# Optimization experiments

Hardware: AMD Instinct MI355X
Metric: run time of the kernel (lower is better)

## Reference

```python
import jax, jax.numpy as jnp
from jax import lax
import numpy as np

# Model dims (from MambaVisionEncoder defaults + HF MambaConfig defaults)
HIDDEN = 128      # hidden_dim
DEPTH = 4         # num_hidden_layers
INTER = 4 * HIDDEN  # intermediate_size = 512
STATE = 16        # state_size
DT_RANK = 8       # ceil(hidden/16)
KCONV = 4         # conv_kernel
EPS = 1e-5        # layer_norm_epsilon
B_, T_ = 2, 256
C_, H_, W_ = 3, 224, 224
INPUT_DIM = C_ * H_ * W_


def setup_inputs() -> dict:
    key = jax.random.key(0)
    ks = jax.random.split(key, 8)
    s = 0.02
    return {
        "x": jax.random.normal(ks[0], (B_, T_, C_, H_, W_), jnp.float32),
        # torch Linear weights are [out, in]
        "project_w": jax.random.normal(ks[1], (HIDDEN, INPUT_DIM), jnp.float32) * s,
        "project_b": jnp.zeros((HIDDEN,), jnp.float32),
        "in_proj_w": jax.random.normal(ks[2], (DEPTH, 2 * INTER, HIDDEN), jnp.float32) * s,
        "conv_w": jax.random.normal(ks[3], (DEPTH, INTER, KCONV), jnp.float32) * s,
        "conv_b": jnp.zeros((DEPTH, INTER), jnp.float32),
        "x_proj_w": jax.random.normal(ks[4], (DEPTH, DT_RANK + 2 * STATE, INTER), jnp.float32) * s,
        "dt_proj_w": jax.random.normal(ks[5], (DEPTH, INTER, DT_RANK), jnp.float32) * s,
        "dt_proj_b": jnp.zeros((DEPTH, INTER), jnp.float32),
        # S4D-style init: A_log = log(1..N), broadcast over channels
        "A_log": jnp.log(jnp.broadcast_to(jnp.arange(1, STATE + 1, dtype=jnp.float32), (DEPTH, INTER, STATE))),
        "D_ssm": jnp.ones((DEPTH, INTER), jnp.float32),
        "out_proj_w": jax.random.normal(ks[6], (DEPTH, HIDDEN, INTER), jnp.float32) * s,
        "norm_w": jnp.ones((DEPTH, HIDDEN), jnp.float32),
        "norm_f_w": jnp.ones((HIDDEN,), jnp.float32),
    }


def rmsnorm(x, w):
    var = jnp.mean(jnp.square(x), axis=-1, keepdims=True)
    return x * lax.rsqrt(var + EPS) * w


def mamba_mixer(h, ipw, cw, cb, xpw, dtw, dtb, A_log, Dp, opw):
    # h: [B, T, D]
    Bsz, T, _ = h.shape
    proj = jnp.einsum('btd,ed->bte', h, ipw)          # [B, T, 2I]
    hs, gate = jnp.split(proj, 2, axis=-1)
    hs = hs.transpose(0, 2, 1)                         # [B, I, T]
    # causal depthwise conv1d, kernel KCONV
    conv = lax.conv_general_dilated(
        hs, cw[:, None, :], (1,), [(KCONV - 1, 0)],
        dimension_numbers=('NCH', 'OIH', 'NCH'), feature_group_count=INTER)
    hs = jax.nn.silu(conv + cb[None, :, None])         # [B, I, T]
    ssm_in = jnp.einsum('bit,ei->bte', hs, xpw)        # [B, T, dt_rank+2N]
    dt, Bm, Cm = jnp.split(ssm_in, [DT_RANK, DT_RANK + STATE], axis=-1)
    dt = jax.nn.softplus(jnp.einsum('btr,ir->bti', dt, dtw) + dtb)  # [B, T, I]
    A = -jnp.exp(A_log)                                # [I, N]
    u = hs.transpose(0, 2, 1)                          # [B, T, I]
    dA = jnp.exp(dt[..., None] * A[None, None])        # [B, T, I, N]
    dBu = dt[..., None] * Bm[:, :, None, :] * u[..., None]  # [B, T, I, N]

    def step(state, inp):                              # state: [B, I, N]
        dA_t, dBu_t, C_t = inp
        state = dA_t * state + dBu_t
        y_t = jnp.einsum('bin,bn->bi', state, C_t)
        return state, y_t

    init = jnp.zeros((Bsz, INTER, STATE), hs.dtype)
    _, ys = lax.scan(step, init, (dA.transpose(1, 0, 2, 3), dBu.transpose(1, 0, 2, 3), Cm.transpose(1, 0, 2)))
    y = ys.transpose(1, 0, 2)                          # [B, T, I]
    y = (y + u * Dp[None, None, :]) * jax.nn.silu(gate)
    return jnp.einsum('bti,di->btd', y, opw)           # [B, T, D]


def reference(x, project_w, project_b, in_proj_w, conv_w, conv_b, x_proj_w,
              dt_proj_w, dt_proj_b, A_log, D_ssm, out_proj_w, norm_w, norm_f_w):
    B, T = x.shape[0], x.shape[1]
    flat = x.reshape(B, T, -1)                         # [B, T, input_dim]
    h = jnp.einsum('bti,di->btd', flat, project_w) + project_b  # [B, T, HIDDEN]
    for l in range(DEPTH):
        h = h + mamba_mixer(rmsnorm(h, norm_w[l]), in_proj_w[l], conv_w[l], conv_b[l],
                            x_proj_w[l], dt_proj_w[l], dt_proj_b[l], A_log[l],
                            D_ssm[l], out_proj_w[l])
    return rmsnorm(h, norm_f_w)
```

## Files before the change

kernel.cpp:

```cpp
#include <hip/hip_runtime.h>
#include <hip/hip_bf16.h>

#define HIDDEN 128
#define DEPTH 4
#define INTER 512
#define NSTATE 16
#define DT_RANK 8
#define EPS_RMS 1e-5f
#define MTOK 512
#define KIN 150528

typedef __attribute__((ext_vector_type(8))) short bf16x8;
typedef __attribute__((ext_vector_type(4))) float f32x4;

__device__ __forceinline__ unsigned short f2bf(float f) {
  unsigned int u = __builtin_bit_cast(unsigned int, f);
  u += 0x7fffu + ((u >> 16) & 1u);
  return (unsigned short)(u >> 16);
}
__device__ __forceinline__ float silu_f(float x) {
  return x / (1.0f + __expf(-x));
}

__global__ __launch_bounds__(256) void zero_part(float* __restrict__ p)
{
  const size_t i = (size_t)blockIdx.x * 256 + threadIdx.x;
  ((float4*)p)[i] = (float4){0.f, 0.f, 0.f, 0.f};
}

__global__ __launch_bounds__(512) void proj_gemm(
    const float* __restrict__ x, const float* __restrict__ w,
    float* __restrict__ partial)
{
  const int bid = blockIdx.x;
  const int mb = (bid >> 3) & 3;
  const int kb = (bid & 7) + (bid >> 5) * 8;
  const int nchunk = 18 + (kb < 24 ? 1 : 0);
  const int c0 = kb * 18 + (kb < 24 ? kb : 24);

  __shared__ char sm[256 * 256];

  const int tid = threadIdx.x;
  const int lane = tid & 63;
  const int wv = tid >> 6;
  const int wm2 = wv >> 2;
  const int wn4 = wv & 3;
  const int fr = lane & 15;
  const int kq = lane >> 4;
  const int l31 = lane & 31;
  const int rpar = lane >> 5;

  const float* gptr = (wv < 4)
      ? (x + (size_t)(mb * 128 + wv * 32 + rpar) * KIN + l31 * 4)
      : (w + (size_t)((wv - 4) * 32 + rpar) * KIN + l31 * 4);

  f32x4 acc[4][2];
  #pragma unroll
  for (int mi = 0; mi < 4; ++mi) {
    acc[mi][0] = (f32x4){0.f, 0.f, 0.f, 0.f};
    acc[mi][1] = (f32x4){0.f, 0.f, 0.f, 0.f};
  }

  float4 rv[16];
  {
    const float* base = gptr + (size_t)c0 * 128;
    #pragma unroll
    for (int j = 0; j < 16; ++j)
      rv[j] = *(const float4*)(base + (size_t)(j * 2) * KIN);
  }

  for (int cc = 0; cc < nchunk; ++cc) {
    #pragma unroll
    for (int j = 0; j < 16; ++j) {
      const int r = wv * 32 + j * 2 + rpar;
      const int phys = (l31 * 8) ^ ((r & 7) << 4);
      ushort4 bq = {f2bf(rv[j].x), f2bf(rv[j].y), f2bf(rv[j].z), f2bf(rv[j].w)};
      *(ushort4*)(sm + r * 256 + phys) = bq;
    }
    __syncthreads();
    if (cc + 1 < nchunk) {
      const float* base = gptr + (size_t)(c0 + cc + 1) * 128;
      #pragma unroll
      for (int j = 0; j < 16; ++j)
        rv[j] = *(const float4*)(base + (size_t)(j * 2) * KIN);
    }
    #pragma unroll
    for (int ks = 0; ks < 4; ++ks) {
      const int log = ks * 64 + kq * 16;
      bf16x8 a[4];
      #pragma unroll
      for (int mi = 0; mi < 4; ++mi) {
        const int row = wm2 * 64 + mi * 16 + fr;
        a[mi] = *(const bf16x8*)(sm + row * 256 + (log ^ ((row & 7) << 4)));
      }
      #pragma unroll
      for (int ni = 0; ni < 2; ++ni) {
        const int row = 128 + wn4 * 32 + ni * 16 + fr;
        const bf16x8 b = *(const bf16x8*)(sm + row * 256 + (log ^ ((row & 7) << 4)));
        #pragma unroll
        for (int mi = 0; mi < 4; ++mi)
          acc[mi][ni] = __builtin_amdgcn_mfma_f32_16x16x32_bf16(a[mi], b, acc[mi][ni], 0, 0, 0);
      }
    }
    __syncthreads();
  }
  float* hp = partial + (size_t)(kb & 15) * (MTOK * HIDDEN);
  #pragma unroll
  for (int mi = 0; mi < 4; ++mi)
    #pragma unroll
    for (int ni = 0; ni < 2; ++ni)
      #pragma unroll
      for (int r = 0; r < 4; ++r) {
        const int row = mb * 128 + wm2 * 64 + mi * 16 + kq * 4 + r;
        const int col = wn4 * 32 + ni * 16 + fr;
        atomicAdd(hp + (size_t)row * HIDDEN + col, acc[mi][ni][r]);
      }
}

__global__ __launch_bounds__(512) void fusedA(
    int mode,
    const float* __restrict__ part, const float* __restrict__ pb,
    const float* __restrict__ y_g, const float* __restrict__ gate_g,
    float* __restrict__ h_g,
    const float* __restrict__ opw,
    const float* __restrict__ nw,
    const float* __restrict__ ipw,
    float* __restrict__ hs_g, float* __restrict__ gate_out,
    float* __restrict__ dout)
{
  const int m0 = blockIdx.x * 2;
  const int tid = threadIdx.x;
  const int o2 = tid >> 1;
  const int half = tid & 1;
  const int t = o2 >> 7, d = o2 & 127;
  __shared__ float y2[2][512];
  __shared__ float hrow[2][128];
  __shared__ float hn[2][128];

  float hv;
  if (mode == 0) {
    hv = pb[d];
    #pragma unroll
    for (int s = 0; s < 16; ++s)
      hv += part[(size_t)s * (MTOK * HIDDEN) + (size_t)(m0 + t) * 128 + d];
  } else {
    #pragma unroll
    for (int j = 0; j < 2; ++j) {
      const int o = tid + j * 512;
      const int tt = o >> 9, i = o & 511;
      const float yv = y_g[(size_t)(m0 + tt) * 512 + i];
      const float g  = gate_g[(size_t)(m0 + tt) * 512 + i];
      y2[tt][i] = yv * silu_f(g);
    }
    __syncthreads();
    const float4* yp = (const float4*)(&y2[t][0] + half * 256);
    const float4* wp = (const float4*)(opw + (size_t)d * 512 + half * 256);
    float a0 = 0.f, a1 = 0.f, a2 = 0.f, a3 = 0.f;
    #pragma unroll 8
    for (int kk = 0; kk < 64; ++kk) {
      const float4 yv = yp[kk], wv4 = wp[kk];
      a0 += yv.x * wv4.x; a1 += yv.y * wv4.y;
      a2 += yv.z * wv4.z; a3 += yv.w * wv4.w;
    }
    float a = (a0 + a1) + (a2 + a3);
    a += __shfl_xor(a, 1);
    hv = h_g[(size_t)(m0 + t) * 128 + d] + a;
  }
  if (mode != 2 && half == 0) h_g[(size_t)(m0 + t) * 128 + d] = hv;
  if (half == 0) hrow[t][d] = hv;
  __syncthreads();
  {
    const int wvi = tid >> 6, ln = tid & 63;
    const int tt = wvi & 1;
    const float v0 = hrow[tt][ln], v1 = hrow[tt][ln + 64];
    float ss = v0 * v0 + v1 * v1;
    #pragma unroll
    for (int off = 1; off < 64; off <<= 1) ss += __shfl_xor(ss, off);
    const float rr = rsqrtf(ss * (1.0f / 128.0f) + EPS_RMS);
    if (mode == 2) {
      if (wvi < 2) {
        dout[(size_t)(m0 + tt) * 128 + ln]      = v0 * rr * nw[ln];
        dout[(size_t)(m0 + tt) * 128 + ln + 64] = v1 * rr * nw[ln + 64];
      }
      return;
    }
    if (wvi < 2) {
      hn[tt][ln]      = v0 * rr * nw[ln];
      hn[tt][ln + 64] = v1 * rr * nw[ln + 64];
    }
  }
  __syncthreads();
  #pragma unroll
  for (int j = 0; j < 4; ++j) {
    const int o = tid + j * 512;
    const int tt = o >> 10, e = o & 1023;
    const float4* hp4 = (const float4*)&hn[tt][0];
    const float4* wp4 = (const float4*)(ipw + (size_t)e * 128);
    float a0 = 0.f, a1 = 0.f, a2 = 0.f, a3 = 0.f;
    #pragma unroll
    for (int kk = 0; kk < 32; ++kk) {
      const float4 hvv = hp4[kk], wv4 = wp4[kk];
      a0 += hvv.x * wv4.x; a1 += hvv.y * wv4.y;
      a2 += hvv.z * wv4.z; a3 += hvv.w * wv4.w;
    }
    const float a = (a0 + a1) + (a2 + a3);
    if (e < 512) hs_g[(size_t)(m0 + tt) * 512 + e] = a;
    else         gate_out[(size_t)(m0 + tt) * 512 + (e - 512)] = a;
  }
}

__global__ __launch_bounds__(512) void convxp(
    const float* __restrict__ hs_g, const float* __restrict__ cw,
    const float* __restrict__ cb, const float* __restrict__ xpw,
    const float* __restrict__ dtw, const float* __restrict__ dtb,
    float* __restrict__ uT, float* __restrict__ dtT,
    float* __restrict__ Bm, float* __restrict__ Cm)
{
  const int m0 = blockIdx.x * 2;
  const int b = m0 >> 8, tb0 = m0 & 255;
  const int tid = threadIdx.x;
  __shared__ float hs5[5][512];
  __shared__ float u4[2][512];
  __shared__ float si[2][40];
  for (int o = tid; o < 2560; o += 512) {
    const int j = o >> 9, i = o & 511;
    const int ct = tb0 - 3 + j;
    hs5[j][i] = (ct >= 0) ? hs_g[((size_t)b * 256 + ct) * 512 + i] : 0.f;
  }
  __syncthreads();
  #pragma unroll
  for (int j = 0; j < 2; ++j) {
    const int o = tid + j * 512;
    const int t = o >> 9, i = o & 511;
    const float4 c4v = *(const float4*)(cw + (size_t)i * 4);
    const float s = cb[i] + c4v.x * hs5[t][i] + c4v.y * hs5[t + 1][i]
                          + c4v.z * hs5[t + 2][i] + c4v.w * hs5[t + 3][i];
    const float uu = silu_f(s);
    u4[t][i] = uu;
    uT[((size_t)b * 512 + i) * 256 + tb0 + t] = uu;
  }
  __syncthreads();
  if (tid < 160) {
    const int pid = tid >> 1, half = tid & 1;
    const int t = pid / 40, e = pid % 40;
    const float4* up = (const float4*)(&u4[t][0] + half * 256);
    const float4* wp = (const float4*)(xpw + (size_t)e * 512 + half * 256);
    float a0 = 0.f, a1 = 0.f, a2 = 0.f, a3 = 0.f;
    #pragma unroll 8
    for (int kk = 0; kk < 64; ++kk) {
      const float4 uv = up[kk], wv4 = wp[kk];
      a0 += uv.x * wv4.x; a1 += uv.y * wv4.y;
      a2 += uv.z * wv4.z; a3 += uv.w * wv4.w;
    }
    float a = (a0 + a1) + (a2 + a3);
    a += __shfl_xor(a, 1);
    if (half == 0) si[t][e] = a;
  }
  __syncthreads();
  if (tid < 64) {
    const int t = tid >> 5, q = tid & 31;
    if (q < 16) Bm[(size_t)(m0 + t) * 16 + q] = si[t][8 + q];
    else        Cm[(size_t)(m0 + t) * 16 + (q - 16)] = si[t][24 + (q - 16)];
  }
  #pragma unroll
  for (int j = 0; j < 2; ++j) {
    const int o = tid + j * 512;
    const int i = o >> 1, t = o & 1;
    float a0 = dtb[i];
    const float* dr = dtw + (size_t)i * 8;
    #pragma unroll
    for (int r = 0; r < 8; ++r) a0 += si[t][r] * dr[r];
    const float sp = (a0 > 20.f) ? a0 : log1pf(__expf(a0));
    dtT[((size_t)b * 512 + i) * 256 + tb0 + t] = sp;
  }
}

__global__ __launch_bounds__(256) void scan_k(
    const float* __restrict__ uT, const float* __restrict__ dtT,
    const float* __restrict__ Bm, const float* __restrict__ Cm,
    const float* __restrict__ Alog, const float* __restrict__ Dssm,
    float* __restrict__ y_g)
{
  const int blk = blockIdx.x;
  const int b = blk >> 9, i = blk & 511;
  const int tid = threadIdx.x;
  __shared__ float dt_r[256], u_r[256];
  __shared__ float B_l[256][17], C_l[256][17];
  __shared__ float e_l[16][17], P_l[16][17];
  dt_r[tid] = dtT[((size_t)b * 512 + i) * 256 + tid];
  u_r[tid]  = uT[((size_t)b * 512 + i) * 256 + tid];
  #pragma unroll
  for (int j = 0; j < 16; ++j) {
    const int o = tid + j * 256;
    B_l[o >> 4][o & 15] = Bm[(size_t)b * 4096 + o];
    C_l[o >> 4][o & 15] = Cm[(size_t)b * 4096 + o];
  }
  __syncthreads();
  const int c = tid >> 4, n = tid & 15;
  const float Av = -__expf(Alog[(size_t)i * 16 + n]);
  const float Dv = Dssm[i];
  float aj[16], xj[16];
  float s = 0.f, P = 1.f;
  #pragma unroll
  for (int j = 0; j < 16; ++j) {
    const int t = c * 16 + j;
    const float dtv = dt_r[t];
    const float a = __expf(Av * dtv);
    const float xx = dtv * B_l[t][n] * u_r[t];
    aj[j] = a; xj[j] = xx;
    s = a * s + xx; P *= a;
  }
  e_l[c][n] = s; P_l[c][n] = P;
  __syncthreads();
  float s0 = 0.f;
  for (int cc = 0; cc < c; ++cc)
    s0 = P_l[cc][n] * s0 + e_l[cc][n];
  s = s0;
  #pragma unroll
  for (int j = 0; j < 16; ++j) {
    const int t = c * 16 + j;
    s = aj[j] * s + xj[j];
    float p = s * C_l[t][n];
    p += __shfl_xor(p, 1); p += __shfl_xor(p, 2);
    p += __shfl_xor(p, 4); p += __shfl_xor(p, 8);
    if (n == 0)
      y_g[((size_t)b * 256 + t) * 512 + i] = p + u_r[t] * Dv;
  }
}

extern "C" void kernel_launch(void* const* d_in, const int* in_sizes, int n_in,
                              void* d_out, int out_size, void* d_ws, size_t ws_size,
                              hipStream_t stream)
{
  (void)in_sizes; (void)n_in; (void)out_size; (void)ws_size;
  const float* x    = (const float*)d_in[0];
  const float* pw   = (const float*)d_in[1];
  const float* pb   = (const float*)d_in[2];
  const float* ipw  = (const float*)d_in[3];
  const float* cw   = (const float*)d_in[4];
  const float* cb   = (const float*)d_in[5];
  const float* xpw  = (const float*)d_in[6];
  const float* dtw  = (const float*)d_in[7];
  const float* dtb  = (const float*)d_in[8];
  const float* Alog = (const float*)d_in[9];
  const float* Dssm = (const float*)d_in[10];
  const float* opw  = (const float*)d_in[11];
  const float* nw   = (const float*)d_in[12];
  const float* nwf  = (const float*)d_in[13];
  float* out = (float*)d_out;

  float* ws   = (float*)d_ws;
  float* part = ws;
  float* h    = part + 16 * 65536;
  float* hs   = h + 65536;
  float* gate = hs + 262144;
  float* uT   = gate + 262144;
  float* dtT  = uT + 262144;
  float* Bm   = dtT + 262144;
  float* Cm   = Bm + 8192;
  float* y    = Cm + 8192;

  zero_part<<<dim3(1024), 256, 0, stream>>>(part);
  proj_gemm<<<dim3(256), 512, 0, stream>>>(x, pw, part);

  fusedA<<<dim3(256), 512, 0, stream>>>(0, part, pb, nullptr, nullptr, h,
                                        nullptr, nw, ipw, hs, gate, nullptr);
  for (int l = 0; l < DEPTH; ++l) {
    convxp<<<dim3(256), 512, 0, stream>>>(
        hs, cw + (size_t)l * 2048, cb + (size_t)l * 512,
        xpw + (size_t)l * 40 * 512, dtw + (size_t)l * 512 * 8,
        dtb + (size_t)l * 512, uT, dtT, Bm, Cm);
    scan_k<<<dim3(1024), 256, 0, stream>>>(
        uT, dtT, Bm, Cm, Alog + (size_t)l * 512 * 16, Dssm + (size_t)l * 512, y);
    if (l < DEPTH - 1)
      fusedA<<<dim3(256), 512, 0, stream>>>(1, nullptr, nullptr, y, gate, h,
          opw + (size_t)l * 128 * 512, nw + (size_t)(l + 1) * 128,
          ipw + (size_t)(l + 1) * 1024 * 128, hs, gate, nullptr);
    else
      fusedA<<<dim3(256), 512, 0, stream>>>(2, nullptr, nullptr, y, gate, h,
          opw + (size_t)l * 128 * 512, nwf, nullptr, nullptr, nullptr, out);
  }
}
```

Before: 415.5 us.

## Fuse per-layer tail kernels into one cooperative persistent kernel with grid syncs

Replaces the sequence of fusedA, convxp and scan_k launches (13 launches) with a single cooperative kernel of 256 blocks that uses grid.sync between stages. The scan stage is remapped so each 512-thread block processes four (batch, channel) units as two 256-thread halves, and it reads B/C directly from global memory into registers instead of staging them in shared memory. The aim is to remove per-launch overhead and idle gaps between small kernels, at the cost of grid-wide barriers and lower parallelism in the scan stage.

```diff
diff --git a/kernel.cpp b/kernel.cpp
--- a/kernel.cpp
+++ b/kernel.cpp
@@ -1,5 +1,8 @@
 #include <hip/hip_runtime.h>
 #include <hip/hip_bf16.h>
+#include <hip/hip_cooperative_groups.h>
+
+namespace cg = cooperative_groups;
 
 #define HIDDEN 128
 #define DEPTH 4
@@ -117,214 +120,273 @@
       }
 }
 
-__global__ __launch_bounds__(512) void fusedA(
-    int mode,
-    const float* __restrict__ part, const float* __restrict__ pb,
-    const float* __restrict__ y_g, const float* __restrict__ gate_g,
-    float* __restrict__ h_g,
-    const float* __restrict__ opw,
-    const float* __restrict__ nw,
-    const float* __restrict__ ipw,
-    float* __restrict__ hs_g, float* __restrict__ gate_out,
-    float* __restrict__ dout)
+struct TailArgs {
+  const float* part; const float* pb;
+  float* h; float* hs; float* gate;
+  float* uT; float* dtT; float* Bm; float* Cm; float* y;
+  float* out;
+  const float* ipw; const float* cw; const float* cb;
+  const float* xpw; const float* dtw; const float* dtb;
+  const float* Alog; const float* Dssm; const float* opw;
+  const float* nw; const float* nwf;
+};
+
+__global__ __launch_bounds__(512) void tail_coop(TailArgs A)
 {
-  const int m0 = blockIdx.x * 2;
+  cg::grid_group grid = cg::this_grid();
+  const int blk = blockIdx.x;
   const int tid = threadIdx.x;
-  const int o2 = tid >> 1;
-  const int half = tid & 1;
-  const int t = o2 >> 7, d = o2 & 127;
-  __shared__ float y2[2][512];
-  __shared__ float hrow[2][128];
-  __shared__ float hn[2][128];
-
-  float hv;
-  if (mode == 0) {
-    hv = pb[d];
+  const int m0 = blk * 2;
+
+  __shared__ __align__(16) char smraw[15360];
+
+  {
+    float* hrow = (float*)smraw;
+    float* hn   = hrow + 256;
+    const int o2 = tid >> 1, half = tid & 1;
+    const int t = o2 >> 7, d = o2 & 127;
+    if (half == 0) {
+      float hv = A.pb[d];
+      #pragma unroll
+      for (int s = 0; s < 16; ++s)
+        hv += A.part[(size_t)s * (MTOK * HIDDEN) + (size_t)(m0 + t) * 128 + d];
+      A.h[(size_t)(m0 + t) * 128 + d] = hv;
+      hrow[t * 128 + d] = hv;
+    }
+    __syncthreads();
+    {
+      const int wvi = tid >> 6, ln = tid & 63;
+      const int tt = wvi & 1;
+      const float v0 = hrow[tt * 128 + ln], v1 = hrow[tt * 128 + ln + 64];
+      float ss = v0 * v0 + v1 * v1;
+      #pragma unroll
+      for (int off = 1; off < 64; off <<= 1) ss += __shfl_xor(ss, off);
+      const float rr = rsqrtf(ss * (1.0f / 128.0f) + EPS_RMS);
+      if (wvi < 2) {
+        hn[tt * 128 + ln]      = v0 * rr * A.nw[ln];
+        hn[tt * 128 + ln + 64] = v1 * rr * A.nw[ln + 64];
+      }
+    }
+    __syncthreads();
     #pragma unroll
-    for (int s = 0; s < 16; ++s)
-      hv += part[(size_t)s * (MTOK * HIDDEN) + (size_t)(m0 + t) * 128 + d];
-  } else {
-    #pragma unroll
-    for (int j = 0; j < 2; ++j) {
+    for (int j = 0; j < 4; ++j) {
       const int o = tid + j * 512;
-      const int tt = o >> 9, i = o & 511;
-      const float yv = y_g[(size_t)(m0 + tt) * 512 + i];
-      const float g  = gate_g[(size_t)(m0 + tt) * 512 + i];
-      y2[tt][i] = yv * silu_f(g);
-    }
-    __syncthreads();
-    const float4* yp = (const float4*)(&y2[t][0] + half * 256);
-    const float4* wp = (const float4*)(opw + (size_t)d * 512 + half * 256);
-    float a0 = 0.f, a1 = 0.f, a2 = 0.f, a3 = 0.f;
-    #pragma unroll 8
-    for (int kk = 0; kk < 64; ++kk) {
-      const float4 yv = yp[kk], wv4 = wp[kk];
-      a0 += yv.x * wv4.x; a1 += yv.y * wv4.y;
-      a2 += yv.z * wv4.z; a3 += yv.w * wv4.w;
-    }
-    float a = (a0 + a1) + (a2 + a3);
-    a += __shfl_xor(a, 1);
-    hv = h_g[(size_t)(m0 + t) * 128 + d] + a;
+      const int tt = o >> 10, e = o & 1023;
+      const float4* hp4 = (const float4*)(hn + tt * 128);
+      const float4* wp4 = (const float4*)(A.ipw + (size_t)e * 128);
+      float a0 = 0.f, a1 = 0.f, a2 = 0.f, a3 = 0.f;
+      #pragma unroll
+      for (int kk = 0; kk < 32; ++kk) {
+        const float4 hvv = hp4[kk], wv4 = wp4[kk];
+        a0 += hvv.x * wv4.x; a1 += hvv.y * wv4.y;
+        a2 += hvv.z * wv4.z; a3 += hvv.w * wv4.w;
+      }
+      const float a = (a0 + a1) + (a2 + a3);
+      if (e < 512) A.hs[(size_t)(m0 + tt) * 512 + e] = a;
+      else         A.gate[(size_t)(m0 + tt) * 512 + (e - 512)] = a;
+    }
   }
-  if (mode != 2 && half == 0) h_g[(size_t)(m0 + t) * 128 + d] = hv;
-  if (half == 0) hrow[t][d] = hv;
-  __syncthreads();
-  {
-    const int wvi = tid >> 6, ln = tid & 63;
-    const int tt = wvi & 1;
-    const float v0 = hrow[tt][ln], v1 = hrow[tt][ln + 64];
-    float ss = v0 * v0 + v1 * v1;
-    #pragma unroll
-    for (int off = 1; off < 64; off <<= 1) ss += __shfl_xor(ss, off);
-    const float rr = rsqrtf(ss * (1.0f / 128.0f) + EPS_RMS);
-    if (mode == 2) {
-      if (wvi < 2) {
-        dout[(size_t)(m0 + tt) * 128 + ln]      = v0 * rr * nw[ln];
-        dout[(size_t)(m0 + tt) * 128 + ln + 64] = v1 * rr * nw[ln + 64];
-      }
-      return;
-    }
-    if (wvi < 2) {
-      hn[tt][ln]      = v0 * rr * nw[ln];
-      hn[tt][ln + 64] = v1 * rr * nw[ln + 64];
-    }
-  }
-  __syncthreads();
-  #pragma unroll
-  for (int j = 0; j < 4; ++j) {
-    const int o = tid + j * 512;
-    const int tt = o >> 10, e = o & 1023;
-    const float4* hp4 = (const float4*)&hn[tt][0];
-    const float4* wp4 = (const float4*)(ipw + (size_t)e * 128);
-    float a0 = 0.f, a1 = 0.f, a2 = 0.f, a3 = 0.f;
-    #pragma unroll
-    for (int kk = 0; kk < 32; ++kk) {
-      const float4 hvv = hp4[kk], wv4 = wp4[kk];
-      a0 += hvv.x * wv4.x; a1 += hvv.y * wv4.y;
-      a2 += hvv.z * wv4.z; a3 += hvv.w * wv4.w;
-    }
-    const float a = (a0 + a1) + (a2 + a3);
-    if (e < 512) hs_g[(size_t)(m0 + tt) * 512 + e] = a;
-    else         gate_out[(size_t)(m0 + tt) * 512 + (e - 512)] = a;
-  }
-}
-
-__global__ __launch_bounds__(512) void convxp(
-    const float* __restrict__ hs_g, const float* __restrict__ cw,
-    const float* __restrict__ cb, const float* __restrict__ xpw,
-    const float* __restrict__ dtw, const float* __restrict__ dtb,
-    float* __restrict__ uT, float* __restrict__ dtT,
-    float* __restrict__ Bm, float* __restrict__ Cm)
-{
-  const int m0 = blockIdx.x * 2;
-  const int b = m0 >> 8, tb0 = m0 & 255;
-  const int tid = threadIdx.x;
-  __shared__ float hs5[5][512];
-  __shared__ float u4[2][512];
-  __shared__ float si[2][40];
-  for (int o = tid; o < 2560; o += 512) {
-    const int j = o >> 9, i = o & 511;
-    const int ct = tb0 - 3 + j;
-    hs5[j][i] = (ct >= 0) ? hs_g[((size_t)b * 256 + ct) * 512 + i] : 0.f;
-  }
-  __syncthreads();
-  #pragma unroll
-  for (int j = 0; j < 2; ++j) {
-    const int o = tid + j * 512;
-    const int t = o >> 9, i = o & 511;
-    const float4 c4v = *(const float4*)(cw + (size_t)i * 4);
-    const float s = cb[i] + c4v.x * hs5[t][i] + c4v.y * hs5[t + 1][i]
-                          + c4v.z * hs5[t + 2][i] + c4v.w * hs5[t + 3][i];
-    const float uu = silu_f(s);
-    u4[t][i] = uu;
-    uT[((size_t)b * 512 + i) * 256 + tb0 + t] = uu;
-  }
-  __syncthreads();
-  if (tid < 160) {
-    const int pid = tid >> 1, half = tid & 1;
-    const int t = pid / 40, e = pid % 40;
-    const float4* up = (const float4*)(&u4[t][0] + half * 256);
-    const float4* wp = (const float4*)(xpw + (size_t)e * 512 + half * 256);
-    float a0 = 0.f, a1 = 0.f, a2 = 0.f, a3 = 0.f;
-    #pragma unroll 8
-    for (int kk = 0; kk < 64; ++kk) {
-      const float4 uv = up[kk], wv4 = wp[kk];
-      a0 += uv.x * wv4.x; a1 += uv.y * wv4.y;
-      a2 += uv.z * wv4.z; a3 += uv.w * wv4.w;
-    }
-    float a = (a0 + a1) + (a2 + a3);
-    a += __shfl_xor(a, 1);
-    if (half == 0) si[t][e] = a;
-  }
-  __syncthreads();
-  if (tid < 64) {
-    const int t = tid >> 5, q = tid & 31;
-    if (q < 16) Bm[(size_t)(m0 + t) * 16 + q] = si[t][8 + q];
-    else        Cm[(size_t)(m0 + t) * 16 + (q - 16)] = si[t][24 + (q - 16)];
-  }
-  #pragma unroll
-  for (int j = 0; j < 2; ++j) {
-    const int o = tid + j * 512;
-    const int i = o >> 1, t = o & 1;
-    float a0 = dtb[i];
-    const float* dr = dtw + (size_t)i * 8;
-    #pragma unroll
-    for (int r = 0; r < 8; ++r) a0 += si[t][r] * dr[r];
-    const float sp = (a0 > 20.f) ? a0 : log1pf(__expf(a0));
-    dtT[((size_t)b * 512 + i) * 256 + tb0 + t] = sp;
-  }
-}
-
-__global__ __launch_bounds__(256) void scan_k(
-    const float* __restrict__ uT, const float* __restrict__ dtT,
-    const float* __restrict__ Bm, const float* __restrict__ Cm,
-    const float* __restrict__ Alog, const float* __restrict__ Dssm,
-    float* __restrict__ y_g)
-{
-  const int blk = blockIdx.x;
-  const int b = blk >> 9, i = blk & 511;
-  const int tid = threadIdx.x;
-  __shared__ float dt_r[256], u_r[256];
-  __shared__ float B_l[256][17], C_l[256][17];
-  __shared__ float e_l[16][17], P_l[16][17];
-  dt_r[tid] = dtT[((size_t)b * 512 + i) * 256 + tid];
-  u_r[tid]  = uT[((size_t)b * 512 + i) * 256 + tid];
-  #pragma unroll
-  for (int j = 0; j < 16; ++j) {
-    const int o = tid + j * 256;
-    B_l[o >> 4][o & 15] = Bm[(size_t)b * 4096 + o];
-    C_l[o >> 4][o & 15] = Cm[(size_t)b * 4096 + o];
-  }
-  __syncthreads();
-  const int c = tid >> 4, n = tid & 15;
-  const float Av = -__expf(Alog[(size_t)i * 16 + n]);
-  const float Dv = Dssm[i];
-  float aj[16], xj[16];
-  float s = 0.f, P = 1.f;
-  #pragma unroll
-  for (int j = 0; j < 16; ++j) {
-    const int t = c * 16 + j;
-    const float dtv = dt_r[t];
-    const float a = __expf(Av * dtv);
-    const float xx = dtv * B_l[t][n] * u_r[t];
-    aj[j] = a; xj[j] = xx;
-    s = a * s + xx; P *= a;
-  }
-  e_l[c][n] = s; P_l[c][n] = P;
-  __syncthreads();
-  float s0 = 0.f;
-  for (int cc = 0; cc < c; ++cc)
-    s0 = P_l[cc][n] * s0 + e_l[cc][n];
-  s = s0;
-  #pragma unroll
-  for (int j = 0; j < 16; ++j) {
-    const int t = c * 16 + j;
-    s = aj[j] * s + xj[j];
-    float p = s * C_l[t][n];
-    p += __shfl_xor(p, 1); p += __shfl_xor(p, 2);
-    p += __shfl_xor(p, 4); p += __shfl_xor(p, 8);
-    if (n == 0)
-      y_g[((size_t)b * 256 + t) * 512 + i] = p + u_r[t] * Dv;
+  grid.sync();
+
+  for (int l = 0; l < DEPTH; ++l) {
+    {
+      float* hs5 = (float*)smraw;
+      float* u4  = hs5 + 2560;
+      float* si  = u4 + 1024;
+      const float* cw  = A.cw  + (size_t)l * 2048;
+      const float* cb  = A.cb  + (size_t)l * 512;
+      const float* xpw = A.xpw + (size_t)l * 40 * 512;
+      const float* dtw = A.dtw + (size_t)l * 512 * 8;
+      const float* dtb = A.dtb + (size_t)l * 512;
+      const int b = m0 >> 8, tb0 = m0 & 255;
+      for (int o = tid; o < 2560; o += 512) {
+        const int j = o >> 9, i = o & 511;
+        const int ct = tb0 - 3 + j;
+        hs5[j * 512 + i] = (ct >= 0) ? A.hs[((size_t)b * 256 + ct) * 512 + i] : 0.f;
+      }
+      __syncthreads();
+      #pragma unroll
+      for (int j = 0; j < 2; ++j) {
+        const int o = tid + j * 512;
+        const int t = o >> 9, i = o & 511;
+        const float4 c4v = *(const float4*)(cw + (size_t)i * 4);
+        const float s = cb[i] + c4v.x * hs5[t * 512 + i] + c4v.y * hs5[(t + 1) * 512 + i]
+                              + c4v.z * hs5[(t + 2) * 512 + i] + c4v.w * hs5[(t + 3) * 512 + i];
+        const float uu = silu_f(s);
+        u4[t * 512 + i] = uu;
+        A.uT[((size_t)b * 512 + i) * 256 + tb0 + t] = uu;
+      }
+      __syncthreads();
+      if (tid < 160) {
+        const int pid = tid >> 1, half = tid & 1;
+        const int t = pid / 40, e = pid % 40;
+        const float4* up = (const float4*)(u4 + t * 512 + half * 256);
+        const float4* wp = (const float4*)(xpw + (size_t)e * 512 + half * 256);
+        float a0 = 0.f, a1 = 0.f, a2 = 0.f, a3 = 0.f;
+        #pragma unroll 8
+        for (int kk = 0; kk < 64; ++kk) {
+          const float4 uv = up[kk], wv4 = wp[kk];
+          a0 += uv.x * wv4.x; a1 += uv.y * wv4.y;
+          a2 += uv.z * wv4.z; a3 += uv.w * wv4.w;
+        }
+        float a = (a0 + a1) + (a2 + a3);
+        a += __shfl_xor(a, 1);
+        if (half == 0) si[t * 40 + e] = a;
+      }
+      __syncthreads();
+      if (tid < 64) {
+        const int t = tid >> 5, q = tid & 31;
+        if (q < 16) A.Bm[(size_t)(m0 + t) * 16 + q] = si[t * 40 + 8 + q];
+        else        A.Cm[(size_t)(m0 + t) * 16 + (q - 16)] = si[t * 40 + 24 + (q - 16)];
+      }
+      #pragma unroll
+      for (int j = 0; j < 2; ++j) {
+        const int o = tid + j * 512;
+        const int i = o >> 1, t = o & 1;
+        float a0 = dtb[i];
+        const float* dr = dtw + (size_t)i * 8;
+        #pragma unroll
+        for (int r = 0; r < 8; ++r) a0 += si[t * 40 + r] * dr[r];
+        const float sp = (a0 > 20.f) ? a0 : log1pf(__expf(a0));
+        A.dtT[((size_t)b * 512 + i) * 256 + tb0 + t] = sp;
+      }
+    }
+    grid.sync();
+
+    {
+      float* dt_l = (float*)smraw;
+      float* u_l  = dt_l + 512;
+      float* e_l  = u_l + 512;
+      float* P_l  = e_l + 544;
+      const float* Alg = A.Alog + (size_t)l * INTER * NSTATE;
+      const float* Dsp = A.Dssm + (size_t)l * INTER;
+      const int sub = tid >> 8;
+      const int t2 = tid & 255;
+      const int c = t2 >> 4, n = t2 & 15;
+      for (int rd = 0; rd < 2; ++rd) {
+        const int unit = blk * 4 + sub * 2 + rd;
+        const int b = unit >> 9, i = unit & 511;
+        dt_l[sub * 256 + t2] = A.dtT[((size_t)b * 512 + i) * 256 + t2];
+        u_l [sub * 256 + t2] = A.uT [((size_t)b * 512 + i) * 256 + t2];
+        const float Av = -__expf(Alg[(size_t)i * 16 + n]);
+        const float Dv = Dsp[i];
+        float Bv[16], Cv[16];
+        #pragma unroll
+        for (int j = 0; j < 16; ++j) {
+          const int t = c * 16 + j;
+          Bv[j] = A.Bm[(size_t)b * 4096 + t * 16 + n];
+          Cv[j] = A.Cm[(size_t)b * 4096 + t * 16 + n];
+        }
+        __syncthreads();
+        float aj[16];
+        float s = 0.f, P = 1.f;
+        #pragma unroll
+        for (int j = 0; j < 16; ++j) {
+          const int t = c * 16 + j;
+          const float dtv = dt_l[sub * 256 + t];
+          const float a = __expf(Av * dtv);
+          aj[j] = a;
+          s = a * s + dtv * Bv[j] * u_l[sub * 256 + t];
+          P *= a;
+        }
+        e_l[sub * 272 + c * 17 + n] = s;
+        P_l[sub * 272 + c * 17 + n] = P;
+        __syncthreads();
+        float s0 = 0.f;
+        for (int cc = 0; cc < c; ++cc)
+          s0 = P_l[sub * 272 + cc * 17 + n] * s0 + e_l[sub * 272 + cc * 17 + n];
+        s = s0;
+        #pragma unroll
+        for (int j = 0; j < 16; ++j) {
+          const int t = c * 16 + j;
+          const float dtv = dt_l[sub * 256 + t];
+          s = aj[j] * s + dtv * Bv[j] * u_l[sub * 256 + t];
+          float p = s * Cv[j];
+          p += __shfl_xor(p, 1); p += __shfl_xor(p, 2);
+          p += __shfl_xor(p, 4); p += __shfl_xor(p, 8);
+          if (n == 0)
+            A.y[((size_t)b * 256 + t) * 512 + i] = p + u_l[sub * 256 + t] * Dv;
+        }
+        __syncthreads();
+      }
+    }
+    grid.sync();
+
+    {
+      float* y2   = (float*)smraw;
+      float* hrow = y2 + 1024;
+      float* hn   = hrow + 256;
+      const float* opw = A.opw + (size_t)l * 128 * 512;
+      const int o2 = tid >> 1, half = tid & 1;
+      const int t = o2 >> 7, d = o2 & 127;
+      #pragma unroll
+      for (int j = 0; j < 2; ++j) {
+        const int o = tid + j * 512;
+        const int tt = o >> 9, i = o & 511;
+        const float yv = A.y[(size_t)(m0 + tt) * 512 + i];
+        const float g  = A.gate[(size_t)(m0 + tt) * 512 + i];
+        y2[tt * 512 + i] = yv * silu_f(g);
+      }
+      __syncthreads();
+      {
+        const float4* yp = (const float4*)(y2 + t * 512 + half * 256);
+        const float4* wp = (const float4*)(opw + (size_t)d * 512 + half * 256);
+        float a0 = 0.f, a1 = 0.f, a2 = 0.f, a3 = 0.f;
+        #pragma unroll 8
+        for (int kk = 0; kk < 64; ++kk) {
+          const float4 yv = yp[kk], wv4 = wp[kk];
+          a0 += yv.x * wv4.x; a1 += yv.y * wv4.y;
+          a2 += yv.z * wv4.z; a3 += yv.w * wv4.w;
+        }
+        float a = (a0 + a1) + (a2 + a3);
+        a += __shfl_xor(a, 1);
+        const float hv = A.h[(size_t)(m0 + t) * 128 + d] + a;
+        if (l < 3 && half == 0) A.h[(size_t)(m0 + t) * 128 + d] = hv;
+        if (half == 0) hrow[t * 128 + d] = hv;
+      }
+      __syncthreads();
+      const float* nwp = (l < 3) ? (A.nw + (size_t)(l + 1) * 128) : A.nwf;
+      {
+        const int wvi = tid >> 6, ln = tid & 63;
+        const int tt = wvi & 1;
+        const float v0 = hrow[tt * 128 + ln], v1 = hrow[tt * 128 + ln + 64];
+        float ss = v0 * v0 + v1 * v1;
+        #pragma unroll
+        for (int off = 1; off < 64; off <<= 1) ss += __shfl_xor(ss, off);
+        const float rr = rsqrtf(ss * (1.0f / 128.0f) + EPS_RMS);
+        if (l == 3) {
+          if (wvi < 2) {
+            A.out[(size_t)(m0 + tt) * 128 + ln]      = v0 * rr * nwp[ln];
+            A.out[(size_t)(m0 + tt) * 128 + ln + 64] = v1 * rr * nwp[ln + 64];
+          }
+        } else if (wvi < 2) {
+          hn[tt * 128 + ln]      = v0 * rr * nwp[ln];
+          hn[tt * 128 + ln + 64] = v1 * rr * nwp[ln + 64];
+        }
+      }
+      if (l < 3) {
+        __syncthreads();
+        const float* ipw = A.ipw + (size_t)(l + 1) * 1024 * 128;
+        #pragma unroll
+        for (int j = 0; j < 4; ++j) {
+          const int o = tid + j * 512;
+          const int tt = o >> 10, e = o & 1023;
+          const float4* hp4 = (const float4*)(hn + tt * 128);
+          const float4* wp4 = (const float4*)(ipw + (size_t)e * 128);
+          float a0 = 0.f, a1 = 0.f, a2 = 0.f, a3 = 0.f;
+          #pragma unroll
+          for (int kk = 0; kk < 32; ++kk) {
+            const float4 hvv = hp4[kk], wv4 = wp4[kk];
+            a0 += hvv.x * wv4.x; a1 += hvv.y * wv4.y;
+            a2 += hvv.z * wv4.z; a3 += hvv.w * wv4.w;
+          }
+          const float a = (a0 + a1) + (a2 + a3);
+          if (e < 512) A.hs[(size_t)(m0 + tt) * 512 + e] = a;
+          else         A.gate[(size_t)(m0 + tt) * 512 + (e - 512)] = a;
+        }
+      }
+    }
+    if (l < 3) grid.sync();
   }
 }
 
@@ -363,21 +425,16 @@
   zero_part<<<dim3(1024), 256, 0, stream>>>(part);
   proj_gemm<<<dim3(256), 512, 0, stream>>>(x, pw, part);
 
-  fusedA<<<dim3(256), 512, 0, stream>>>(0, part, pb, nullptr, nullptr, h,
-                                        nullptr, nw, ipw, hs, gate, nullptr);
-  for (int l = 0; l < DEPTH; ++l) {
-    convxp<<<dim3(256), 512, 0, stream>>>(
-        hs, cw + (size_t)l * 2048, cb + (size_t)l * 512,
-        xpw + (size_t)l * 40 * 512, dtw + (size_t)l * 512 * 8,
-        dtb + (size_t)l * 512, uT, dtT, Bm, Cm);
-    scan_k<<<dim3(1024), 256, 0, stream>>>(
-        uT, dtT, Bm, Cm, Alog + (size_t)l * 512 * 16, Dssm + (size_t)l * 512, y);
-    if (l < DEPTH - 1)
-      fusedA<<<dim3(256), 512, 0, stream>>>(1, nullptr, nullptr, y, gate, h,
-          opw + (size_t)l * 128 * 512, nw + (size_t)(l + 1) * 128,
-          ipw + (size_t)(l + 1) * 1024 * 128, hs, gate, nullptr);
-    else
-      fusedA<<<dim3(256), 512, 0, stream>>>(2, nullptr, nullptr, y, gate, h,
-          opw + (size_t)l * 128 * 512, nwf, nullptr, nullptr, nullptr, out);
-  }
-}
+  TailArgs ta;
+  ta.part = part; ta.pb = pb;
+  ta.h = h; ta.hs = hs; ta.gate = gate;
+  ta.uT = uT; ta.dtT = dtT; ta.Bm = Bm; ta.Cm = Cm; ta.y = y;
+  ta.out = out;
+  ta.ipw = ipw; ta.cw = cw; ta.cb = cb;
+  ta.xpw = xpw; ta.dtw = dtw; ta.dtb = dtb;
+  ta.Alog = Alog; ta.Dssm = Dssm; ta.opw = opw;
+  ta.nw = nw; ta.nwf = nwf;
+  void* kargs[] = { &ta };
+  hipLaunchCooperativeKernel((const void*)tail_coop, dim3(256), dim3(512),
+                             kargs, 0, stream);
+}
```

Result: slower. 725.7 us (+74.7%).
